# Kernel optimization log

Hardware: AMD Instinct MI355X
Metric: run time of the kernel (lower is better)

Reference implementation:

```python
import jax, jax.numpy as jnp
import numpy as np

DIM = 1024
NUM_HEADS = 16
D_HEAD = DIM // NUM_HEADS  # 64
N_SEQ = 1605               # 1600 patch tokens + 5 prefix (cls+registers)
HW = 1600


def setup_inputs() -> dict:
    key = jax.random.key(0)
    kx, kr, kq, kp, kb = jax.random.split(key, 5)
    x = jax.random.normal(kx, (N_SEQ, DIM), dtype=jnp.float32)
    # rope = stack([sin, cos]) of per-position, per-channel angles
    angles = jax.random.uniform(kr, (HW, D_HEAD), dtype=jnp.float32) * (2.0 * np.pi)
    rope = jnp.stack([jnp.sin(angles), jnp.cos(angles)], axis=0)  # [2, hw, d_head]
    W_qkv = jax.random.normal(kq, (3 * DIM, DIM), dtype=jnp.float32)
    W_proj = jax.random.normal(kp, (DIM, DIM), dtype=jnp.float32)
    b_proj = jax.random.normal(kb, (DIM,), dtype=jnp.float32)
    return {"x": x, "rope": rope, "W_qkv": W_qkv, "W_proj": W_proj, "b_proj": b_proj}


def _rope_apply(t, sin, cos):
    # t: [hw, n_head, d_head]; sin/cos: [hw, d_head]
    half = t.shape[-1] // 2
    rot = jnp.concatenate([-t[..., half:], t[..., :half]], axis=-1)  # rotate_half
    return t * cos[:, None, :] + rot * sin[:, None, :]


def reference(x, rope, W_qkv, W_proj, b_proj):
    n_seq = x.shape[0]
    qkv = x @ W_qkv.T                                   # [n_seq, 3*dim]
    qkv = qkv.reshape(n_seq, 3, NUM_HEADS, D_HEAD)
    q, k, v = qkv[:, 0], qkv[:, 1], qkv[:, 2]           # [n_seq, nh, dh]
    sin, cos = rope[0], rope[1]
    prefix = n_seq - sin.shape[0]
    q = jnp.concatenate([q[:prefix], _rope_apply(q[prefix:], sin, cos)], axis=0)
    k = jnp.concatenate([k[:prefix], _rope_apply(k[prefix:], sin, cos)], axis=0)
    scale = 1.0 / np.sqrt(D_HEAD)
    scores = jnp.einsum("qhd,khd->hqk", q, k) * scale   # [nh, n_seq, n_seq]
    attn = jax.nn.softmax(scores, axis=-1)
    out = jnp.einsum("hqk,khd->qhd", attn, v)           # [n_seq, nh, dh]
    out = out.reshape(n_seq, DIM)
    return out @ W_proj.T + b_proj
```

## Files before the change

kernel.cpp:

```cpp
#include <hip/hip_runtime.h>
#include <hip/hip_bf16.h>

#define DIM    1024
#define NH     16
#define DH     64
#define NSEQ   1605
#define HWIN   1600
#define PREFIX 5
#define NSEQP  1664
#define KX     3072

typedef __bf16 bf16_t;
typedef bf16_t bf16x4 __attribute__((ext_vector_type(4)));
typedef bf16_t bf16x8 __attribute__((ext_vector_type(8)));
typedef float  f32x4  __attribute__((ext_vector_type(4)));
typedef unsigned short u16;

#define MFMA(a,b,c) __builtin_amdgcn_mfma_f32_16x16x32_bf16(a,b,c,0,0,0)

union BU { bf16_t b; u16 u; };

template<int ROWS>
__device__ __forceinline__ void stage64(const bf16_t* __restrict__ seg,
                                        int row0, int ldk, int kin,
                                        bf16_t* lds, int tid)
{
    const int l = tid & 63, w = tid >> 6;
#pragma unroll
    for (int i = 0; i < ROWS / 32; ++i) {
        const int rb = i * 32 + w * 8;
        const int r  = rb + (l >> 3);
        const int p  = l & 7;
        const bf16_t* src = seg + (size_t)(row0 + r) * ldk + kin + ((p ^ (r & 7)) << 3);
        __builtin_amdgcn_global_load_lds(
            (const __attribute__((address_space(1))) void*)src,
            (__attribute__((address_space(3))) void*)(lds + rb * 64),
            16, 0, 0);
    }
}

__device__ __forceinline__ bf16x8 frag(const bf16_t* lds, int row, int ch) {
    return *(const bf16x8*)&lds[row * 64 + ((ch ^ (row & 7)) << 3)];
}

#define NX4 (NSEQP * 256)
#define NQ4 (3072 * 256)
#define NP4 (1024 * 256)

__global__ __launch_bounds__(256) void prep_kernel(
    const float* __restrict__ x, const float* __restrict__ Wq,
    const float* __restrict__ Wp,
    bf16_t* __restrict__ xh, bf16_t* __restrict__ xl,
    bf16_t* __restrict__ wqh, bf16_t* __restrict__ wql,
    bf16_t* __restrict__ wph, bf16_t* __restrict__ wpl)
{
    const int i = blockIdx.x * 256 + threadIdx.x;
    if (i >= NX4 + NQ4 + NP4) return;
    float4 v = make_float4(0.f, 0.f, 0.f, 0.f);
    bf16_t *ph, *pl;
    size_t off;
    if (i < NX4) {
        if ((i >> 8) < NSEQ) v = ((const float4*)x)[i];
        ph = xh; pl = xl; off = (size_t)i * 4;
    } else if (i < NX4 + NQ4) {
        int j = i - NX4;
        v = ((const float4*)Wq)[j];
        ph = wqh; pl = wql; off = (size_t)j * 4;
    } else {
        int j = i - NX4 - NQ4;
        v = ((const float4*)Wp)[j];
        ph = wph; pl = wpl; off = (size_t)j * 4;
    }
    bf16_t h0 = (bf16_t)v.x, h1 = (bf16_t)v.y, h2 = (bf16_t)v.z, h3 = (bf16_t)v.w;
    bf16x4 hv = {h0, h1, h2, h3};
    bf16x4 lv = {(bf16_t)(v.x - (float)h0), (bf16_t)(v.y - (float)h1),
                 (bf16_t)(v.z - (float)h2), (bf16_t)(v.w - (float)h3)};
    *(bf16x4*)(ph + off) = hv;
    *(bf16x4*)(pl + off) = lv;
}

__global__ __launch_bounds__(256, 2) void gemm_qkv(
    const bf16_t* __restrict__ xh, const bf16_t* __restrict__ xl,
    const bf16_t* __restrict__ wqh, const bf16_t* __restrict__ wql,
    const float* __restrict__ rope,
    bf16_t* __restrict__ Qhi, bf16_t* __restrict__ Qlo,
    bf16_t* __restrict__ Khi, bf16_t* __restrict__ Klo,
    bf16_t* __restrict__ Vt)
{
    __shared__ bf16_t As[128 * 64];
    __shared__ bf16_t Bs[128 * 64];

    const int lin = blockIdx.y * 24 + blockIdx.x;
    const int swz = (lin & 7) * 39 + (lin >> 3);
    const int m0 = (swz / 24) * 128, n0 = (swz % 24) * 128;

    const int tid = threadIdx.x;
    const int w = tid >> 6, l = tid & 63, lr = l & 15, lg = l >> 4;
    const int wr = (w >> 1) * 64, wc = (w & 1) * 64;

    f32x4 acc[4][4] = {};

    for (int kt = 0; kt < KX / 64; ++kt) {
        const int k0 = kt * 64, sg = k0 >> 10, kin = k0 & 1023;
        const bf16_t* Aseg = (sg == 1) ? xl : xh;
        const bf16_t* Bseg = (sg == 2) ? wql : wqh;
        stage64<128>(Aseg, m0, 1024, kin, As, tid);
        stage64<128>(Bseg, n0, 1024, kin, Bs, tid);
        __syncthreads();
#pragma unroll
        for (int ks = 0; ks < 2; ++ks) {
            bf16x8 a[4];
#pragma unroll
            for (int rt = 0; rt < 4; ++rt) a[rt] = frag(As, wr + 16 * rt + lr, ks * 4 + lg);
#pragma unroll
            for (int ct = 0; ct < 4; ++ct) {
                bf16x8 b = frag(Bs, wc + 16 * ct + lr, ks * 4 + lg);
#pragma unroll
                for (int rt = 0; rt < 4; ++rt)
                    acc[rt][ct] = MFMA(a[rt], b, acc[rt][ct]);
            }
        }
        __syncthreads();
    }

    const int which = n0 >> 10;
    const int cbase = (n0 & 1023) + wc;
    const float qscale = (which == 0) ? 0.125f : 1.0f;
    const float* sinp = rope;
    const float* cosp = rope + (size_t)HWIN * DH;

#pragma unroll
    for (int ct = 0; ct < 4; ++ct) {
        const int col = cbase + 16 * ct + lr;
        const int hd = col >> 6, dd = col & 63;
#pragma unroll
        for (int rt = 0; rt < 4; ++rt) {
            const int sbase = m0 + wr + 16 * rt + 4 * lg;
            if (sbase >= NSEQ) continue;
            if (which == 2) {
                size_t off = ((size_t)hd * DH + dd) * NSEQP + sbase;
                if (sbase + 3 < NSEQ) {
                    BU t0, t1, t2, t3;
                    t0.b = (bf16_t)acc[rt][ct][0]; t1.b = (bf16_t)acc[rt][ct][1];
                    t2.b = (bf16_t)acc[rt][ct][2]; t3.b = (bf16_t)acc[rt][ct][3];
                    *(ushort4*)((u16*)Vt + off) = make_ushort4(t0.u, t1.u, t2.u, t3.u);
                } else {
#pragma unroll
                    for (int reg = 0; reg < 4; ++reg)
                        if (sbase + reg < NSEQ)
                            Vt[off + reg] = (bf16_t)acc[rt][ct][reg];
                }
            } else {
#pragma unroll
                for (int reg = 0; reg < 4; ++reg) {
                    const int seq = sbase + reg;
                    if (seq >= NSEQ) continue;
                    float val = acc[rt][ct][reg] * qscale;
                    float o = val;
                    if (seq >= PREFIX) {
                        float partner = acc[rt][ct ^ 2][reg] * qscale;
                        float rot = (dd < 32) ? -partner : partner;
                        float sn = sinp[(size_t)(seq - PREFIX) * DH + dd];
                        float cs = cosp[(size_t)(seq - PREFIX) * DH + dd];
                        o = val * cs + rot * sn;
                    }
                    bf16_t hh = (bf16_t)o;
                    bf16_t ll = (bf16_t)(o - (float)hh);
                    size_t off = ((size_t)hd * NSEQP + seq) * DH + dd;
                    if (which == 0) { Qhi[off] = hh; Qlo[off] = ll; }
                    else            { Khi[off] = hh; Klo[off] = ll; }
                }
            }
        }
    }
}

#define ASTRH 72

__global__ __launch_bounds__(256, 2) void attn_kernel(
    const bf16_t* __restrict__ Qhi, const bf16_t* __restrict__ Qlo,
    const bf16_t* __restrict__ Khi, const bf16_t* __restrict__ Klo,
    const bf16_t* __restrict__ Vt,
    bf16_t* __restrict__ Oh, bf16_t* __restrict__ Ol)
{
    __shared__ bf16_t Ksh[64 * 64], Ksl[64 * 64], Vsh[64 * 64];
    __shared__ bf16_t PS[4][16 * ASTRH];

    const int lin = blockIdx.y * 26 + blockIdx.x;
    const int swz = (lin & 7) * 52 + (lin >> 3);
    const int h = swz / 26, q0 = (swz % 26) * 64;

    const int tid = threadIdx.x, w = tid >> 6, l = tid & 63;
    const int lr = l & 15, lg = l >> 4;

    bf16x8 qh[2], ql[2];
    {
        const size_t qoff = ((size_t)h * NSEQP + q0 + 16 * w + lr) * DH;
#pragma unroll
        for (int ks = 0; ks < 2; ++ks) {
            qh[ks] = *(const bf16x8*)&Qhi[qoff + 32 * ks + 8 * lg];
            ql[ks] = *(const bf16x8*)&Qlo[qoff + 32 * ks + 8 * lg];
        }
    }

    const bf16_t* KbH = Khi + (size_t)h * NSEQP * DH;
    const bf16_t* KbL = Klo + (size_t)h * NSEQP * DH;
    const bf16_t* Vb  = Vt  + (size_t)h * DH * NSEQP;

    f32x4 o[4] = {};
    float m[4], lsum[4];
#pragma unroll
    for (int r = 0; r < 4; ++r) { m[r] = -1e30f; lsum[r] = 0.f; }

    for (int j0 = 0; j0 < NSEQ; j0 += 64) {
        stage64<64>(KbH, j0, 64, 0, Ksh, tid);
        stage64<64>(KbL, j0, 64, 0, Ksl, tid);
        stage64<64>(Vb, 0, NSEQP, j0, Vsh, tid);
        __syncthreads();

        f32x4 s[4] = {};
        __builtin_amdgcn_s_setprio(1);
#pragma unroll
        for (int ct = 0; ct < 4; ++ct) {
#pragma unroll
            for (int ks = 0; ks < 2; ++ks) {
                bf16x8 bh = frag(Ksh, 16 * ct + lr, ks * 4 + lg);
                bf16x8 bl = frag(Ksl, 16 * ct + lr, ks * 4 + lg);
                s[ct] = MFMA(ql[ks], bh, s[ct]);
                s[ct] = MFMA(qh[ks], bl, s[ct]);
                s[ct] = MFMA(qh[ks], bh, s[ct]);
            }
        }
        __builtin_amdgcn_s_setprio(0);
#pragma unroll
        for (int ct = 0; ct < 4; ++ct) {
            if (j0 + 16 * ct + lr >= NSEQ) {
                s[ct][0] = -1e30f; s[ct][1] = -1e30f;
                s[ct][2] = -1e30f; s[ct][3] = -1e30f;
            }
        }

        float so[4];
#pragma unroll
        for (int reg = 0; reg < 4; ++reg) {
            float mt = fmaxf(fmaxf(s[0][reg], s[1][reg]), fmaxf(s[2][reg], s[3][reg]));
#pragma unroll
            for (int off = 1; off < 16; off <<= 1)
                mt = fmaxf(mt, __shfl_xor(mt, off));
            float mn = fmaxf(m[reg], mt);
            so[reg] = __expf(m[reg] - mn);
            m[reg] = mn;
            float psum = 0.f;
#pragma unroll
            for (int ct = 0; ct < 4; ++ct) {
                float pv = __expf(s[ct][reg] - mn);
                s[ct][reg] = pv;
                psum += pv;
            }
#pragma unroll
            for (int off = 1; off < 16; off <<= 1)
                psum += __shfl_xor(psum, off);
            lsum[reg] = lsum[reg] * so[reg] + psum;
        }

#pragma unroll
        for (int ct = 0; ct < 4; ++ct)
#pragma unroll
            for (int reg = 0; reg < 4; ++reg)
                PS[w][(4 * lg + reg) * ASTRH + 16 * ct + lr] = (bf16_t)s[ct][reg];

#pragma unroll
        for (int ctd = 0; ctd < 4; ++ctd)
#pragma unroll
            for (int reg = 0; reg < 4; ++reg)
                o[ctd][reg] *= so[reg];

        __builtin_amdgcn_s_setprio(1);
#pragma unroll
        for (int ks = 0; ks < 2; ++ks) {
            bf16x8 pa = *(const bf16x8*)&PS[w][lr * ASTRH + 32 * ks + 8 * lg];
#pragma unroll
            for (int ctd = 0; ctd < 4; ++ctd) {
                bf16x8 vb = frag(Vsh, 16 * ctd + lr, ks * 4 + lg);
                o[ctd] = MFMA(pa, vb, o[ctd]);
            }
        }
        __builtin_amdgcn_s_setprio(0);
        __syncthreads();
    }

#pragma unroll
    for (int ctd = 0; ctd < 4; ++ctd) {
#pragma unroll
        for (int reg = 0; reg < 4; ++reg) {
            const int seq = q0 + 16 * w + 4 * lg + reg;
            if (seq < NSEQ) {
                float ov = o[ctd][reg] / lsum[reg];
                bf16_t hi = (bf16_t)ov;
                bf16_t lo = (bf16_t)(ov - (float)hi);
                size_t oo = (size_t)seq * DIM + h * DH + 16 * ctd + lr;
                Oh[oo] = hi; Ol[oo] = lo;
            }
        }
    }
}

__global__ __launch_bounds__(256, 2) void gemm_proj(
    const bf16_t* __restrict__ oh, const bf16_t* __restrict__ ol,
    const bf16_t* __restrict__ wph, const bf16_t* __restrict__ wpl,
    const float* __restrict__ bias, float* __restrict__ C)
{
    __shared__ bf16_t As[64 * 64];
    __shared__ bf16_t Bs[128 * 64];

    const int lin = blockIdx.y * 8 + blockIdx.x;
    const int swz = (lin & 7) * 26 + (lin >> 3);
    const int m0 = (swz / 8) * 64, n0 = (swz % 8) * 128;

    const int tid = threadIdx.x;
    const int w = tid >> 6, l = tid & 63, lr = l & 15, lg = l >> 4;
    const int wr = (w >> 1) * 32, wc = (w & 1) * 64;

    f32x4 acc[2][4] = {};

    for (int kt = 0; kt < KX / 64; ++kt) {
        const int k0 = kt * 64, sg = k0 >> 10, kin = k0 & 1023;
        const bf16_t* Aseg = (sg == 1) ? ol : oh;
        const bf16_t* Bseg = (sg == 2) ? wpl : wph;
        stage64<64>(Aseg, m0, 1024, kin, As, tid);
        stage64<128>(Bseg, n0, 1024, kin, Bs, tid);
        __syncthreads();
#pragma unroll
        for (int ks = 0; ks < 2; ++ks) {
            bf16x8 a[2];
#pragma unroll
            for (int rt = 0; rt < 2; ++rt) a[rt] = frag(As, wr + 16 * rt + lr, ks * 4 + lg);
#pragma unroll
            for (int ct = 0; ct < 4; ++ct) {
                bf16x8 b = frag(Bs, wc + 16 * ct + lr, ks * 4 + lg);
#pragma unroll
                for (int rt = 0; rt < 2; ++rt)
                    acc[rt][ct] = MFMA(a[rt], b, acc[rt][ct]);
            }
        }
        __syncthreads();
    }

#pragma unroll
    for (int ct = 0; ct < 4; ++ct) {
        const int n = n0 + wc + 16 * ct + lr;
        const float bv = bias[n];
#pragma unroll
        for (int rt = 0; rt < 2; ++rt) {
#pragma unroll
            for (int reg = 0; reg < 4; ++reg) {
                const int seq = m0 + wr + 16 * rt + 4 * lg + reg;
                if (seq < NSEQ)
                    C[(size_t)seq * DIM + n] = acc[rt][ct][reg] + bv;
            }
        }
    }
}

extern "C" void kernel_launch(void* const* d_in, const int* in_sizes, int n_in,
                              void* d_out, int out_size, void* d_ws, size_t ws_size,
                              hipStream_t stream)
{
    const float* x     = (const float*)d_in[0];
    const float* rope  = (const float*)d_in[1];
    const float* Wqkv  = (const float*)d_in[2];
    const float* Wproj = (const float*)d_in[3];
    const float* bproj = (const float*)d_in[4];
    float* out = (float*)d_out;

    const size_t XE  = (size_t)NSEQP * 1024;
    const size_t WQE = (size_t)3072 * 1024;
    const size_t WPE = (size_t)1024 * 1024;
    const size_t HSE = (size_t)NH * NSEQP * DH;

    bf16_t* p = (bf16_t*)d_ws;
    bf16_t* xh  = p; p += XE;
    bf16_t* xl  = p; p += XE;
    bf16_t* wqh = p; p += WQE;
    bf16_t* wql = p; p += WQE;
    bf16_t* wph = p; p += WPE;
    bf16_t* wpl = p; p += WPE;
    bf16_t* Qhi = p; p += HSE;
    bf16_t* Qlo = p; p += HSE;
    bf16_t* Khi = p; p += HSE;
    bf16_t* Klo = p; p += HSE;
    bf16_t* Vt  = p; p += HSE;
    bf16_t* Oh  = xh;
    bf16_t* Ol  = xl;

    const int PTOT = NX4 + NQ4 + NP4;
    prep_kernel<<<(PTOT + 255) / 256, 256, 0, stream>>>(
        x, Wqkv, Wproj, xh, xl, wqh, wql, wph, wpl);

    gemm_qkv<<<dim3(KX / 128, NSEQP / 128), 256, 0, stream>>>(
        xh, xl, wqh, wql, rope, Qhi, Qlo, Khi, Klo, Vt);

    attn_kernel<<<dim3(NSEQP / 64, NH), 256, 0, stream>>>(
        Qhi, Qlo, Khi, Klo, Vt, Oh, Ol);

    gemm_proj<<<dim3(DIM / 128, NSEQP / 64), 256, 0, stream>>>(
        Oh, Ol, wph, wpl, bproj, out);
}
```

Before: 245.0 us.

## Double-buffer LDS staging in all kernels, shrink GEMM tiles, remap blocks per XCD

All three kernels now stage tiles into two LDS buffers and prefetch the next K or KV tile while computing on the current one, keeping a single barrier per iteration. The QKV GEMM tile shrinks from 128x128 to 64x128 and the projection GEMM from 64x128 to 64x64, doubling the grid for better CU fill. Block-to-tile mapping is changed so each XCD handles a contiguous set of N columns or heads to improve L2 locality. The cost is more LDS per block and smaller per-block reuse.

Result: faster. 224.6 us (-8.3%).

```diff
diff --git a/kernel.cpp b/kernel.cpp
--- a/kernel.cpp
+++ b/kernel.cpp
@@ -87,40 +87,48 @@
     bf16_t* __restrict__ Khi, bf16_t* __restrict__ Klo,
     bf16_t* __restrict__ Vt)
 {
-    __shared__ bf16_t As[128 * 64];
-    __shared__ bf16_t Bs[128 * 64];
+    __shared__ bf16_t As[2][64 * 64];
+    __shared__ bf16_t Bs[2][128 * 64];
 
     const int lin = blockIdx.y * 24 + blockIdx.x;
-    const int swz = (lin & 7) * 39 + (lin >> 3);
-    const int m0 = (swz / 24) * 128, n0 = (swz % 24) * 128;
+    const int xcd = lin & 7, idx = lin >> 3;
+    const int m0 = (idx / 3) * 64;
+    const int n0 = (xcd * 3 + idx % 3) * 128;
 
     const int tid = threadIdx.x;
     const int w = tid >> 6, l = tid & 63, lr = l & 15, lg = l >> 4;
-    const int wr = (w >> 1) * 64, wc = (w & 1) * 64;
-
-    f32x4 acc[4][4] = {};
-
-    for (int kt = 0; kt < KX / 64; ++kt) {
+    const int wr = (w >> 1) * 32, wc = (w & 1) * 64;
+
+    f32x4 acc[2][4] = {};
+
+    auto stage = [&](int buf, int kt) {
         const int k0 = kt * 64, sg = k0 >> 10, kin = k0 & 1023;
         const bf16_t* Aseg = (sg == 1) ? xl : xh;
         const bf16_t* Bseg = (sg == 2) ? wql : wqh;
-        stage64<128>(Aseg, m0, 1024, kin, As, tid);
-        stage64<128>(Bseg, n0, 1024, kin, Bs, tid);
+        stage64<64>(Aseg, m0, 1024, kin, As[buf], tid);
+        stage64<128>(Bseg, n0, 1024, kin, Bs[buf], tid);
+    };
+
+    stage(0, 0);
+    __syncthreads();
+    int cur = 0;
+    for (int kt = 0; kt < KX / 64; ++kt) {
+        if (kt + 1 < KX / 64) stage(cur ^ 1, kt + 1);
+#pragma unroll
+        for (int ks = 0; ks < 2; ++ks) {
+            bf16x8 a[2];
+#pragma unroll
+            for (int rt = 0; rt < 2; ++rt) a[rt] = frag(As[cur], wr + 16 * rt + lr, ks * 4 + lg);
+#pragma unroll
+            for (int ct = 0; ct < 4; ++ct) {
+                bf16x8 b = frag(Bs[cur], wc + 16 * ct + lr, ks * 4 + lg);
+#pragma unroll
+                for (int rt = 0; rt < 2; ++rt)
+                    acc[rt][ct] = MFMA(a[rt], b, acc[rt][ct]);
+            }
+        }
         __syncthreads();
-#pragma unroll
-        for (int ks = 0; ks < 2; ++ks) {
-            bf16x8 a[4];
-#pragma unroll
-            for (int rt = 0; rt < 4; ++rt) a[rt] = frag(As, wr + 16 * rt + lr, ks * 4 + lg);
-#pragma unroll
-            for (int ct = 0; ct < 4; ++ct) {
-                bf16x8 b = frag(Bs, wc + 16 * ct + lr, ks * 4 + lg);
-#pragma unroll
-                for (int rt = 0; rt < 4; ++rt)
-                    acc[rt][ct] = MFMA(a[rt], b, acc[rt][ct]);
-            }
-        }
-        __syncthreads();
+        cur ^= 1;
     }
 
     const int which = n0 >> 10;
@@ -134,7 +142,7 @@
         const int col = cbase + 16 * ct + lr;
         const int hd = col >> 6, dd = col & 63;
 #pragma unroll
-        for (int rt = 0; rt < 4; ++rt) {
+        for (int rt = 0; rt < 2; ++rt) {
             const int sbase = m0 + wr + 16 * rt + 4 * lg;
             if (sbase >= NSEQ) continue;
             if (which == 2) {
@@ -176,6 +184,7 @@
 }
 
 #define ASTRH 72
+#define NJT   (NSEQP / 64)
 
 __global__ __launch_bounds__(256, 2) void attn_kernel(
     const bf16_t* __restrict__ Qhi, const bf16_t* __restrict__ Qlo,
@@ -183,12 +192,13 @@
     const bf16_t* __restrict__ Vt,
     bf16_t* __restrict__ Oh, bf16_t* __restrict__ Ol)
 {
-    __shared__ bf16_t Ksh[64 * 64], Ksl[64 * 64], Vsh[64 * 64];
+    __shared__ bf16_t Ksh[2][64 * 64], Ksl[2][64 * 64], Vsh[2][64 * 64];
     __shared__ bf16_t PS[4][16 * ASTRH];
 
     const int lin = blockIdx.y * 26 + blockIdx.x;
-    const int swz = (lin & 7) * 52 + (lin >> 3);
-    const int h = swz / 26, q0 = (swz % 26) * 64;
+    const int xcd = lin & 7, idx = lin >> 3;
+    const int h = 2 * xcd + idx / 26;
+    const int q0 = (idx % 26) * 64;
 
     const int tid = threadIdx.x, w = tid >> 6, l = tid & 63;
     const int lr = l & 15, lg = l >> 4;
@@ -212,11 +222,19 @@
 #pragma unroll
     for (int r = 0; r < 4; ++r) { m[r] = -1e30f; lsum[r] = 0.f; }
 
-    for (int j0 = 0; j0 < NSEQ; j0 += 64) {
-        stage64<64>(KbH, j0, 64, 0, Ksh, tid);
-        stage64<64>(KbL, j0, 64, 0, Ksl, tid);
-        stage64<64>(Vb, 0, NSEQP, j0, Vsh, tid);
-        __syncthreads();
+    auto stage_kv = [&](int buf, int jt) {
+        const int j0 = jt * 64;
+        stage64<64>(KbH, j0, 64, 0, Ksh[buf], tid);
+        stage64<64>(KbL, j0, 64, 0, Ksl[buf], tid);
+        stage64<64>(Vb, 0, NSEQP, j0, Vsh[buf], tid);
+    };
+
+    stage_kv(0, 0);
+    __syncthreads();
+    int cur = 0;
+    for (int jt = 0; jt < NJT; ++jt) {
+        const int j0 = jt * 64;
+        if (jt + 1 < NJT) stage_kv(cur ^ 1, jt + 1);
 
         f32x4 s[4] = {};
         __builtin_amdgcn_s_setprio(1);
@@ -224,8 +242,8 @@
         for (int ct = 0; ct < 4; ++ct) {
 #pragma unroll
             for (int ks = 0; ks < 2; ++ks) {
-                bf16x8 bh = frag(Ksh, 16 * ct + lr, ks * 4 + lg);
-                bf16x8 bl = frag(Ksl, 16 * ct + lr, ks * 4 + lg);
+                bf16x8 bh = frag(Ksh[cur], 16 * ct + lr, ks * 4 + lg);
+                bf16x8 bl = frag(Ksl[cur], 16 * ct + lr, ks * 4 + lg);
                 s[ct] = MFMA(ql[ks], bh, s[ct]);
                 s[ct] = MFMA(qh[ks], bl, s[ct]);
                 s[ct] = MFMA(qh[ks], bh, s[ct]);
@@ -281,12 +299,14 @@
             bf16x8 pa = *(const bf16x8*)&PS[w][lr * ASTRH + 32 * ks + 8 * lg];
 #pragma unroll
             for (int ctd = 0; ctd < 4; ++ctd) {
-                bf16x8 vb = frag(Vsh, 16 * ctd + lr, ks * 4 + lg);
+                bf16x8 vb = frag(Vsh[cur], 16 * ctd + lr, ks * 4 + lg);
                 o[ctd] = MFMA(pa, vb, o[ctd]);
             }
         }
         __builtin_amdgcn_s_setprio(0);
+
         __syncthreads();
+        cur ^= 1;
     }
 
 #pragma unroll
@@ -310,44 +330,52 @@
     const bf16_t* __restrict__ wph, const bf16_t* __restrict__ wpl,
     const float* __restrict__ bias, float* __restrict__ C)
 {
-    __shared__ bf16_t As[64 * 64];
-    __shared__ bf16_t Bs[128 * 64];
-
-    const int lin = blockIdx.y * 8 + blockIdx.x;
-    const int swz = (lin & 7) * 26 + (lin >> 3);
-    const int m0 = (swz / 8) * 64, n0 = (swz % 8) * 128;
+    __shared__ bf16_t As[2][64 * 64];
+    __shared__ bf16_t Bs[2][64 * 64];
+
+    const int lin = blockIdx.y * 16 + blockIdx.x;
+    const int xcd = lin & 7, idx = lin >> 3;
+    const int m0 = (idx >> 1) * 64;
+    const int n0 = ((xcd << 1) | (idx & 1)) * 64;
 
     const int tid = threadIdx.x;
     const int w = tid >> 6, l = tid & 63, lr = l & 15, lg = l >> 4;
-    const int wr = (w >> 1) * 32, wc = (w & 1) * 64;
-
-    f32x4 acc[2][4] = {};
-
-    for (int kt = 0; kt < KX / 64; ++kt) {
+    const int wr = (w >> 1) * 32, wc = (w & 1) * 32;
+
+    f32x4 acc[2][2] = {};
+
+    auto stage = [&](int buf, int kt) {
         const int k0 = kt * 64, sg = k0 >> 10, kin = k0 & 1023;
         const bf16_t* Aseg = (sg == 1) ? ol : oh;
         const bf16_t* Bseg = (sg == 2) ? wpl : wph;
-        stage64<64>(Aseg, m0, 1024, kin, As, tid);
-        stage64<128>(Bseg, n0, 1024, kin, Bs, tid);
-        __syncthreads();
+        stage64<64>(Aseg, m0, 1024, kin, As[buf], tid);
+        stage64<64>(Bseg, n0, 1024, kin, Bs[buf], tid);
+    };
+
+    stage(0, 0);
+    __syncthreads();
+    int cur = 0;
+    for (int kt = 0; kt < KX / 64; ++kt) {
+        if (kt + 1 < KX / 64) stage(cur ^ 1, kt + 1);
 #pragma unroll
         for (int ks = 0; ks < 2; ++ks) {
             bf16x8 a[2];
 #pragma unroll
-            for (int rt = 0; rt < 2; ++rt) a[rt] = frag(As, wr + 16 * rt + lr, ks * 4 + lg);
-#pragma unroll
-            for (int ct = 0; ct < 4; ++ct) {
-                bf16x8 b = frag(Bs, wc + 16 * ct + lr, ks * 4 + lg);
+            for (int rt = 0; rt < 2; ++rt) a[rt] = frag(As[cur], wr + 16 * rt + lr, ks * 4 + lg);
+#pragma unroll
+            for (int ct = 0; ct < 2; ++ct) {
+                bf16x8 b = frag(Bs[cur], wc + 16 * ct + lr, ks * 4 + lg);
 #pragma unroll
                 for (int rt = 0; rt < 2; ++rt)
                     acc[rt][ct] = MFMA(a[rt], b, acc[rt][ct]);
             }
         }
         __syncthreads();
-    }
-
-#pragma unroll
-    for (int ct = 0; ct < 4; ++ct) {
+        cur ^= 1;
+    }
+
+#pragma unroll
+    for (int ct = 0; ct < 2; ++ct) {
         const int n = n0 + wc + 16 * ct + lr;
         const float bv = bias[n];
 #pragma unroll
@@ -397,12 +425,12 @@
     prep_kernel<<<(PTOT + 255) / 256, 256, 0, stream>>>(
         x, Wqkv, Wproj, xh, xl, wqh, wql, wph, wpl);
 
-    gemm_qkv<<<dim3(KX / 128, NSEQP / 128), 256, 0, stream>>>(
+    gemm_qkv<<<dim3(24, NSEQP / 64), 256, 0, stream>>>(
         xh, xl, wqh, wql, rope, Qhi, Qlo, Khi, Klo, Vt);
 
-    attn_kernel<<<dim3(NSEQP / 64, NH), 256, 0, stream>>>(
+    attn_kernel<<<dim3(26, NH), 256, 0, stream>>>(
         Qhi, Qlo, Khi, Klo, Vt, Oh, Ol);
 
-    gemm_proj<<<dim3(DIM / 128, NSEQP / 64), 256, 0, stream>>>(
+    gemm_proj<<<dim3(16, NSEQP / 64), 256, 0, stream>>>(
         Oh, Ol, wph, wpl, bproj, out);
 }
```
